# Optimization experiments

Hardware: AMD Instinct MI355X
Metric: run time of the kernel (lower is better)

## Reference

```python
import jax, jax.numpy as jnp
import numpy as np

N, D, E, TOP_K = 16384, 1024, 8, 2

def setup_inputs() -> dict:
    key = jax.random.key(0)
    ks = jax.random.split(key, 8)
    sc = 1.0 / np.sqrt(D)
    return {
        "x": jax.random.normal(ks[0], (N, D), dtype=jnp.float32),
        "context_vector": jax.random.uniform(ks[1], (E,), dtype=jnp.float32),
        "router_w": jax.random.uniform(ks[2], (E, D), minval=-sc, maxval=sc),
        "router_b": jax.random.uniform(ks[3], (E,), minval=-sc, maxval=sc),
        "expert_w": jax.random.uniform(ks[4], (E, D, D), minval=-sc, maxval=sc),
        "expert_b": jax.random.uniform(ks[5], (E, D), minval=-sc, maxval=sc),
        "context_weight": jax.random.uniform(ks[6], (1,), dtype=jnp.float32),
    }

def reference(x, context_vector, router_w, router_b, expert_w, expert_b, context_weight):
    # Router: gate logits with conceptual context bias. [N, E]
    gate_logits = x @ router_w.T + router_b + context_weight * context_vector
    weights = jax.nn.softmax(gate_logits, axis=-1)

    # Top-k selection and renormalization. [N, k]
    top_k_weights, top_k_indices = jax.lax.top_k(weights, TOP_K)
    top_k_weights = top_k_weights / jnp.sum(top_k_weights, axis=-1, keepdims=True)

    # All-expert outputs (dense grouped GEMM): y[n,e,:] = x[n] @ W[e].T + b[e]
    all_out = jnp.einsum('nd,efd->nef', x, expert_w) + expert_b  # [N, E, D]

    # Gather the top-k expert outputs per token and combine. [N, k, D]
    gathered = jnp.take_along_axis(all_out, top_k_indices[:, :, None], axis=1)
    expert_outputs = jnp.sum(top_k_weights[:, :, None] * gathered, axis=1)  # [N, D]

    # Load-balancing loss: avg router prob . fraction of tokens routed per expert
    avg_router_prob = weights.mean(axis=0)  # [E]
    assignment_mask = jax.nn.one_hot(top_k_indices, E).sum(axis=1)  # [N, E]
    fraction_routed = assignment_mask.mean(axis=0)  # [E]
    load_loss = jnp.sum(avg_router_prob * fraction_routed)

    return expert_outputs, load_loss
```

## Files before the change

### kernel.cpp

```cpp
#include <hip/hip_runtime.h>
#include <stdint.h>

#define N_TOK 16384
#define DDIM  1024
#define NEXP  8
#define CNT_STRIDE 64

#define BM 128
#define BN 128
#define BK 32

typedef __bf16 bf16x8 __attribute__((ext_vector_type(8)));
typedef float  f32x4  __attribute__((ext_vector_type(4)));

__device__ __forceinline__ unsigned short f2bf(float f) {
  union { float f; uint32_t u; } a; a.f = f;
  uint32_t u = a.u;
  u += 0x7fffu + ((u >> 16) & 1u);
  return (unsigned short)(u >> 16);
}

__device__ __forceinline__ float bf2f(unsigned short u) {
  union { uint32_t u; float f; } a; a.u = ((uint32_t)u) << 16;
  return a.f;
}

__device__ __forceinline__ void load_lds16(const void* g, void* l) {
  __builtin_amdgcn_global_load_lds(
      (const __attribute__((address_space(1))) void*)g,
      (__attribute__((address_space(3))) void*)l,
      16, 0, 0);
}

__global__ __launch_bounds__(256) void cast_w_kernel(const float4* __restrict__ src,
                                                     ushort4* __restrict__ dst) {
  size_t i = (size_t)blockIdx.x * 256 + threadIdx.x;
  float4 v = src[i];
  dst[i] = make_ushort4(f2bf(v.x), f2bf(v.y), f2bf(v.z), f2bf(v.w));
}

__global__ __launch_bounds__(256) void router_kernel(
    const float* __restrict__ x, const float* __restrict__ rw,
    const float* __restrict__ rb, const float* __restrict__ cv,
    const float* __restrict__ cwp,
    unsigned short* __restrict__ xg,
    int* __restrict__ perm_idx, float* __restrict__ perm_w,
    int* __restrict__ inv_idx,
    int* __restrict__ cnt, float* __restrict__ sum_w)
{
  __shared__ int   sCnt[NEXP];
  __shared__ int   sBase[NEXP];
  __shared__ float sSW[NEXP];
  __shared__ int   sE0[32], sE1[32], sR0[32], sR1[32];
  __shared__ float sW0[32], sW1[32];

  const int tid = threadIdx.x;
  if (tid < NEXP) { sCnt[tid] = 0; sSW[tid] = 0.0f; }
  __syncthreads();

  const int wave = tid >> 6;
  const int lane = tid & 63;

  float lsw[NEXP];
#pragma unroll
  for (int e = 0; e < NEXP; ++e) lsw[e] = 0.0f;

  const float cw = cwp[0];

  for (int t = 0; t < 8; ++t) {
    const int i = wave * 8 + t;
    const int n = blockIdx.x * 32 + i;

    float p[NEXP];
#pragma unroll
    for (int e = 0; e < NEXP; ++e) p[e] = 0.0f;

    const float2* x2 = (const float2*)(x + (size_t)n * DDIM);
    uint32_t* xgp = (uint32_t*)(xg + (size_t)n * DDIM);

    float2 xv[8];
#pragma unroll
    for (int it = 0; it < 8; ++it) xv[it] = x2[lane + 64 * it];
#pragma unroll
    for (int it = 0; it < 8; ++it) {
      int dp = lane + 64 * it;
      xgp[dp] = (uint32_t)f2bf(xv[it].x) | ((uint32_t)f2bf(xv[it].y) << 16);
#pragma unroll
      for (int e = 0; e < NEXP; ++e) {
        float2 wv = ((const float2*)(rw + e * DDIM))[dp];
        p[e] = fmaf(xv[it].x, wv.x, fmaf(xv[it].y, wv.y, p[e]));
      }
    }
#pragma unroll
    for (int e = 0; e < NEXP; ++e) {
#pragma unroll
      for (int off = 32; off > 0; off >>= 1)
        p[e] += __shfl_xor(p[e], off, 64);
    }

    if (lane == 0) {
      float w[NEXP];
      float m = -1e30f;
#pragma unroll
      for (int e = 0; e < NEXP; ++e) {
        w[e] = p[e] + rb[e] + cw * cv[e];
        m = fmaxf(m, w[e]);
      }
      float s = 0.0f;
#pragma unroll
      for (int e = 0; e < NEXP; ++e) { w[e] = expf(w[e] - m); s += w[e]; }
      float inv = 1.0f / s;
#pragma unroll
      for (int e = 0; e < NEXP; ++e) { w[e] *= inv; lsw[e] += w[e]; }
      int e0 = 0;
#pragma unroll
      for (int e = 1; e < NEXP; ++e) if (w[e] > w[e0]) e0 = e;
      int e1 = (e0 == 0) ? 1 : 0;
#pragma unroll
      for (int e = 0; e < NEXP; ++e) if (e != e0 && w[e] > w[e1]) e1 = e;
      float rsum = 1.0f / (w[e0] + w[e1]);
      int r0 = atomicAdd(&sCnt[e0], 1);
      int r1 = atomicAdd(&sCnt[e1], 1);
      sE0[i] = e0; sE1[i] = e1; sR0[i] = r0; sR1[i] = r1;
      sW0[i] = w[e0] * rsum; sW1[i] = w[e1] * rsum;
    }
  }

  if (lane == 0) {
#pragma unroll
    for (int e = 0; e < NEXP; ++e) atomicAdd(&sSW[e], lsw[e]);
  }
  __syncthreads();

  if (tid < NEXP) {
    sBase[tid] = atomicAdd(&cnt[tid * CNT_STRIDE], sCnt[tid]);
    atomicAdd(&sum_w[tid * CNT_STRIDE], sSW[tid]);
  }
  __syncthreads();

  if (tid < 64) {
    int i = tid >> 1, k = tid & 1;
    int e = k ? sE1[i] : sE0[i];
    int r = k ? sR1[i] : sR0[i];
    float wv = k ? sW1[i] : sW0[i];
    int pos = sBase[e] + r;
    int n = blockIdx.x * 32 + i;
    perm_idx[e * N_TOK + pos] = n;
    perm_w [e * N_TOK + pos] = wv;
    inv_idx[2 * n + k] = (e << 14) | pos;
  }
}

template<int MODE>
__global__ __launch_bounds__(256) void moe_gemm_kernel(
    const unsigned short* __restrict__ xg, const unsigned short* __restrict__ wb,
    const float* __restrict__ eb,
    const int* __restrict__ perm_idx, const float* __restrict__ perm_w,
    const int* __restrict__ cnt,
    unsigned short* __restrict__ ybuf, float* __restrict__ out)
{
  const int e = blockIdx.z;
  const int count = cnt[e * CNT_STRIDE];
  const int tm = blockIdx.x;
  if (tm * BM >= count) return;
  const int tn = blockIdx.y;

  __shared__ alignas(16) __bf16 As[BM * BK];
  __shared__ alignas(16) __bf16 Bs[BN * BK];
  __shared__ int   tokS[BM];
  __shared__ float wtS[BM];

  const int tid = threadIdx.x;
  const int wave = tid >> 6;
  const int lane = tid & 63;

  if (tid < BM) {
    int row = tm * BM + tid;
    int rc = row < count ? row : count - 1;
    tokS[tid] = perm_idx[e * N_TOK + rc];
    wtS[tid] = (row < count) ? perm_w[e * N_TOK + row] : 0.0f;
  }
  __syncthreads();

  const int slot = lane & 3;
  const int ar0 = wave * 32 + (lane >> 2);
  const int ar1 = ar0 + 16;
  const int ac0 = slot ^ ((ar0 >> 1) & 3);
  const int ac1 = slot ^ ((ar1 >> 1) & 3);

  const unsigned short* aptr0 = xg + (size_t)tokS[ar0] * DDIM + ac0 * 8;
  const unsigned short* aptr1 = xg + (size_t)tokS[ar1] * DDIM + ac1 * 8;
  const unsigned short* wbase = wb + (size_t)e * DDIM * DDIM;
  const unsigned short* bptr0 = wbase + (size_t)(tn * BN + ar0) * DDIM + ac0 * 8;
  const unsigned short* bptr1 = wbase + (size_t)(tn * BN + ar1) * DDIM + ac1 * 8;

  __bf16* aw0 = &As[(wave * 32) * BK];
  __bf16* aw1 = &As[(wave * 32 + 16) * BK];
  __bf16* bw0 = &Bs[(wave * 32) * BK];
  __bf16* bw1 = &Bs[(wave * 32 + 16) * BK];

  const int mw = (wave >> 1) * 64;
  const int nw = (wave & 1) * 64;
  const int quad = lane >> 4;
  const int l15 = lane & 15;

  f32x4 acc[4][4] = {};

  for (int kk = 0; kk < DDIM; kk += BK) {
    load_lds16(aptr0, aw0);
    load_lds16(aptr1, aw1);
    load_lds16(bptr0, bw0);
    load_lds16(bptr1, bw1);
    aptr0 += BK; aptr1 += BK; bptr0 += BK; bptr1 += BK;
    __syncthreads();

    bf16x8 af[4], bfr[4];
#pragma unroll
    for (int mi = 0; mi < 4; ++mi) {
      int m = mw + mi * 16 + l15;
      int pos = quad ^ ((m >> 1) & 3);
      af[mi] = *(const bf16x8*)&As[m * BK + pos * 8];
    }
#pragma unroll
    for (int ni = 0; ni < 4; ++ni) {
      int nn = nw + ni * 16 + l15;
      int pos = quad ^ ((nn >> 1) & 3);
      bfr[ni] = *(const bf16x8*)&Bs[nn * BK + pos * 8];
    }
#pragma unroll
    for (int mi = 0; mi < 4; ++mi)
#pragma unroll
      for (int ni = 0; ni < 4; ++ni)
        acc[mi][ni] = __builtin_amdgcn_mfma_f32_16x16x32_bf16(af[mi], bfr[ni], acc[mi][ni], 0, 0, 0);
    __syncthreads();
  }

  int ebase = 0;
  if (MODE == 1) {
#pragma unroll
    for (int j = 0; j < NEXP; ++j) if (j < e) ebase += cnt[j * CNT_STRIDE];
  }

  const int valid = count - tm * BM;
#pragma unroll
  for (int ni = 0; ni < 4; ++ni) {
    int col = tn * BN + nw + ni * 16 + l15;
    float bias = eb[e * DDIM + col];
#pragma unroll
    for (int mi = 0; mi < 4; ++mi) {
#pragma unroll
      for (int r = 0; r < 4; ++r) {
        int mrow = mw + mi * 16 + quad * 4 + r;
        if (mrow < valid) {
          float v = (acc[mi][ni][r] + bias) * wtS[mrow];
          if (MODE == 1) {
            ybuf[(size_t)(ebase + tm * BM + mrow) * DDIM + col] = f2bf(v);
          } else {
            atomicAdd(out + (size_t)tokS[mrow] * DDIM + col, v);
          }
        }
      }
    }
  }
}

__global__ __launch_bounds__(256) void combine_kernel(
    const unsigned short* __restrict__ ybuf, const int* __restrict__ inv_idx,
    const int* __restrict__ cnt, float* __restrict__ out)
{
  const int wave = threadIdx.x >> 6;
  const int lane = threadIdx.x & 63;
  const int n = blockIdx.x * 4 + wave;

  int base[NEXP];
  int acc = 0;
#pragma unroll
  for (int j = 0; j < NEXP; ++j) { base[j] = acc; acc += cnt[j * CNT_STRIDE]; }

  int i0 = inv_idx[2 * n];
  int i1 = inv_idx[2 * n + 1];
  int g0 = base[i0 >> 14] + (i0 & 16383);
  int g1 = base[i1 >> 14] + (i1 & 16383);

  const ushort4* r0 = (const ushort4*)(ybuf + (size_t)g0 * DDIM);
  const ushort4* r1 = (const ushort4*)(ybuf + (size_t)g1 * DDIM);
  float4* o = (float4*)(out + (size_t)n * DDIM);

#pragma unroll
  for (int it = 0; it < 4; ++it) {
    int c = lane + 64 * it;
    ushort4 a = r0[c];
    ushort4 b = r1[c];
    float4 v;
    v.x = bf2f(a.x) + bf2f(b.x);
    v.y = bf2f(a.y) + bf2f(b.y);
    v.z = bf2f(a.z) + bf2f(b.z);
    v.w = bf2f(a.w) + bf2f(b.w);
    o[c] = v;
  }
}

__global__ void loss_kernel(const float* __restrict__ sum_w,
                            const int* __restrict__ cnt,
                            float* __restrict__ out) {
  if (threadIdx.x == 0 && blockIdx.x == 0) {
    float l = 0.0f;
#pragma unroll
    for (int e = 0; e < NEXP; ++e)
      l += sum_w[e * CNT_STRIDE] * (float)cnt[e * CNT_STRIDE];
    out[(size_t)N_TOK * DDIM] = l * (1.0f / ((float)N_TOK * (float)N_TOK));
  }
}

extern "C" void kernel_launch(void* const* d_in, const int* in_sizes, int n_in,
                              void* d_out, int out_size, void* d_ws, size_t ws_size,
                              hipStream_t stream) {
  const float* x  = (const float*)d_in[0];
  const float* cv = (const float*)d_in[1];
  const float* rw = (const float*)d_in[2];
  const float* rb = (const float*)d_in[3];
  const float* ew = (const float*)d_in[4];
  const float* eb = (const float*)d_in[5];
  const float* cw = (const float*)d_in[6];
  float* out = (float*)d_out;

  char* ws = (char*)d_ws;
  unsigned short* xg = (unsigned short*)ws;
  unsigned short* wb = (unsigned short*)(ws + 33554432);
  int*   perm_idx = (int*)  (ws + 50331648);
  float* perm_w   = (float*)(ws + 50855936);
  int*   inv_idx  = (int*)  (ws + 51380224);
  int*   cnt      = (int*)  (ws + 51511296);
  float* sum_w    = (float*)(ws + 51513344);
  unsigned short* ybuf = (unsigned short*)(ws + 51515392);
  const size_t NEED = 51515392ull + 67108864ull;

  const bool big = ws_size >= NEED;

  hipMemsetAsync(cnt, 0, 4096, stream);
  if (!big)
    hipMemsetAsync(d_out, 0, (size_t)N_TOK * DDIM * sizeof(float), stream);

  cast_w_kernel<<<(NEXP * DDIM * DDIM / 4) / 256, 256, 0, stream>>>(
      (const float4*)ew, (ushort4*)wb);

  router_kernel<<<N_TOK / 32, 256, 0, stream>>>(x, rw, rb, cv, cw,
                                                xg, perm_idx, perm_w, inv_idx, cnt, sum_w);

  if (big) {
    moe_gemm_kernel<1><<<dim3(N_TOK / BM, DDIM / BN, NEXP), 256, 0, stream>>>(
        xg, wb, eb, perm_idx, perm_w, cnt, ybuf, out);
    combine_kernel<<<N_TOK / 4, 256, 0, stream>>>(ybuf, inv_idx, cnt, out);
  } else {
    moe_gemm_kernel<0><<<dim3(N_TOK / BM, DDIM / BN, NEXP), 256, 0, stream>>>(
        xg, wb, eb, perm_idx, perm_w, cnt, ybuf, out);
  }

  loss_kernel<<<1, 64, 0, stream>>>(sum_w, cnt, out);
}
```

Baseline: 321.9 us.

## Fuse weight cast into router, compact GEMM grid, BK=64, LDS-staged epilogue

Folds the expert-weight fp32→bf16 cast into the router kernel, which now runs 512 threads per block, so one launch is removed. The GEMM drops the 3D grid, where most blocks exited early, for a 1D grid over a prefix sum of per-expert tile counts. It also doubles BK to 64 with a new 8-way XOR swizzle, which halves the barrier count. The epilogue stages bf16 results in LDS for 16-byte coalesced stores, and the combine kernel uses wider 16-byte loads. The risks are higher LDS use, possible occupancy loss, and a MAX_TILES bound that assumes at most 264 M-tiles.

```diff
diff --git a/kernel.cpp b/kernel.cpp
--- a/kernel.cpp
+++ b/kernel.cpp
@@ -8,7 +8,9 @@
 
 #define BM 128
 #define BN 128
-#define BK 32
+#define BK 64
+#define MAX_TILES 264
+#define EP_PITCH 72
 
 typedef __bf16 bf16x8 __attribute__((ext_vector_type(8)));
 typedef float  f32x4  __attribute__((ext_vector_type(4)));
@@ -25,6 +27,12 @@
   return a.f;
 }
 
+__device__ __forceinline__ float2 bfpair(uint32_t u) {
+  union { uint32_t u; float f; } lo, hi;
+  lo.u = u << 16; hi.u = u & 0xffff0000u;
+  return make_float2(lo.f, hi.f);
+}
+
 __device__ __forceinline__ void load_lds16(const void* g, void* l) {
   __builtin_amdgcn_global_load_lds(
       (const __attribute__((address_space(1))) void*)g,
@@ -32,17 +40,11 @@
       16, 0, 0);
 }
 
-__global__ __launch_bounds__(256) void cast_w_kernel(const float4* __restrict__ src,
-                                                     ushort4* __restrict__ dst) {
-  size_t i = (size_t)blockIdx.x * 256 + threadIdx.x;
-  float4 v = src[i];
-  dst[i] = make_ushort4(f2bf(v.x), f2bf(v.y), f2bf(v.z), f2bf(v.w));
-}
-
-__global__ __launch_bounds__(256) void router_kernel(
+__global__ __launch_bounds__(512) void router_kernel(
     const float* __restrict__ x, const float* __restrict__ rw,
     const float* __restrict__ rb, const float* __restrict__ cv,
     const float* __restrict__ cwp,
+    const float4* __restrict__ ew4, ushort4* __restrict__ wb4,
     unsigned short* __restrict__ xg,
     int* __restrict__ perm_idx, float* __restrict__ perm_w,
     int* __restrict__ inv_idx,
@@ -67,8 +69,8 @@
 
   const float cw = cwp[0];
 
-  for (int t = 0; t < 8; ++t) {
-    const int i = wave * 8 + t;
+  for (int t = 0; t < 4; ++t) {
+    const int i = wave * 4 + t;
     const int n = blockIdx.x * 32 + i;
 
     float p[NEXP];
@@ -149,6 +151,14 @@
     perm_w [e * N_TOK + pos] = wv;
     inv_idx[2 * n + k] = (e << 14) | pos;
   }
+
+  size_t base = (size_t)blockIdx.x * 512 + tid;
+#pragma unroll
+  for (int i2 = 0; i2 < 8; ++i2) {
+    size_t idx = base + (size_t)i2 * 262144;
+    float4 v = ew4[idx];
+    wb4[idx] = make_ushort4(f2bf(v.x), f2bf(v.y), f2bf(v.z), f2bf(v.w));
+  }
 }
 
 template<int MODE>
@@ -159,14 +169,25 @@
     const int* __restrict__ cnt,
     unsigned short* __restrict__ ybuf, float* __restrict__ out)
 {
-  const int e = blockIdx.z;
-  const int count = cnt[e * CNT_STRIDE];
-  const int tm = blockIdx.x;
-  if (tm * BM >= count) return;
-  const int tn = blockIdx.y;
-
-  __shared__ alignas(16) __bf16 As[BM * BK];
-  __shared__ alignas(16) __bf16 Bs[BN * BK];
+  const int id = blockIdx.x;
+  const int tn = id / MAX_TILES;
+  const int tileIdx = id - tn * MAX_TILES;
+
+  int e = -1, tm = 0, count = 0, ebase = 0, pref = 0;
+#pragma unroll
+  for (int j = 0; j < NEXP; ++j) {
+    int c = cnt[j * CNT_STRIDE];
+    int t = (c + BM - 1) >> 7;
+    if (e < 0 && tileIdx < pref + t) { e = j; tm = tileIdx - pref; count = c; }
+    if (e < 0) ebase += c;
+    pref += t;
+  }
+  if (e < 0) return;
+
+  __shared__ union {
+    struct { __bf16 As[BM * BK]; __bf16 Bs[BN * BK]; } g;
+    __bf16 ep[4 * 64 * EP_PITCH];
+  } sm;
   __shared__ int   tokS[BM];
   __shared__ float wtS[BM];
 
@@ -182,22 +203,16 @@
   }
   __syncthreads();
 
-  const int slot = lane & 3;
-  const int ar0 = wave * 32 + (lane >> 2);
-  const int ar1 = ar0 + 16;
-  const int ac0 = slot ^ ((ar0 >> 1) & 3);
-  const int ac1 = slot ^ ((ar1 >> 1) & 3);
-
-  const unsigned short* aptr0 = xg + (size_t)tokS[ar0] * DDIM + ac0 * 8;
-  const unsigned short* aptr1 = xg + (size_t)tokS[ar1] * DDIM + ac1 * 8;
+  const unsigned short* aptr[4];
+  const unsigned short* bptr[4];
   const unsigned short* wbase = wb + (size_t)e * DDIM * DDIM;
-  const unsigned short* bptr0 = wbase + (size_t)(tn * BN + ar0) * DDIM + ac0 * 8;
-  const unsigned short* bptr1 = wbase + (size_t)(tn * BN + ar1) * DDIM + ac1 * 8;
-
-  __bf16* aw0 = &As[(wave * 32) * BK];
-  __bf16* aw1 = &As[(wave * 32 + 16) * BK];
-  __bf16* bw0 = &Bs[(wave * 32) * BK];
-  __bf16* bw1 = &Bs[(wave * 32 + 16) * BK];
+#pragma unroll
+  for (int t = 0; t < 4; ++t) {
+    int r = wave * 32 + t * 8 + (lane >> 3);
+    int cg = (lane & 7) ^ (r & 7);
+    aptr[t] = xg + (size_t)tokS[r] * DDIM + cg * 8;
+    bptr[t] = wbase + (size_t)(tn * BN + r) * DDIM + cg * 8;
+  }
 
   const int mw = (wave >> 1) * 64;
   const int nw = (wave & 1) * 64;
@@ -207,57 +222,81 @@
   f32x4 acc[4][4] = {};
 
   for (int kk = 0; kk < DDIM; kk += BK) {
-    load_lds16(aptr0, aw0);
-    load_lds16(aptr1, aw1);
-    load_lds16(bptr0, bw0);
-    load_lds16(bptr1, bw1);
-    aptr0 += BK; aptr1 += BK; bptr0 += BK; bptr1 += BK;
+#pragma unroll
+    for (int t = 0; t < 4; ++t) {
+      load_lds16(aptr[t], &sm.g.As[(wave * 32 + t * 8) * BK]);
+      load_lds16(bptr[t], &sm.g.Bs[(wave * 32 + t * 8) * BK]);
+      aptr[t] += BK; bptr[t] += BK;
+    }
     __syncthreads();
 
-    bf16x8 af[4], bfr[4];
+#pragma unroll
+    for (int ks = 0; ks < 2; ++ks) {
+      bf16x8 af[4], bfr[4];
+#pragma unroll
+      for (int mi = 0; mi < 4; ++mi) {
+        int m = mw + mi * 16 + l15;
+        int slot = (ks * 4 + quad) ^ (m & 7);
+        af[mi] = *(const bf16x8*)&sm.g.As[m * BK + slot * 8];
+      }
+#pragma unroll
+      for (int ni = 0; ni < 4; ++ni) {
+        int n = nw + ni * 16 + l15;
+        int slot = (ks * 4 + quad) ^ (n & 7);
+        bfr[ni] = *(const bf16x8*)&sm.g.Bs[n * BK + slot * 8];
+      }
+#pragma unroll
+      for (int mi = 0; mi < 4; ++mi)
+#pragma unroll
+        for (int ni = 0; ni < 4; ++ni)
+          acc[mi][ni] = __builtin_amdgcn_mfma_f32_16x16x32_bf16(bfr[ni], af[mi], acc[mi][ni], 0, 0, 0);
+    }
+    __syncthreads();
+  }
+
+  const int valid = count - tm * BM;
+
+  if (MODE == 1) {
+    __bf16* slab = &sm.ep[wave * (64 * EP_PITCH)];
 #pragma unroll
     for (int mi = 0; mi < 4; ++mi) {
-      int m = mw + mi * 16 + l15;
-      int pos = quad ^ ((m >> 1) & 3);
-      af[mi] = *(const bf16x8*)&As[m * BK + pos * 8];
-    }
-#pragma unroll
-    for (int ni = 0; ni < 4; ++ni) {
-      int nn = nw + ni * 16 + l15;
-      int pos = quad ^ ((nn >> 1) & 3);
-      bfr[ni] = *(const bf16x8*)&Bs[nn * BK + pos * 8];
-    }
-#pragma unroll
-    for (int mi = 0; mi < 4; ++mi)
-#pragma unroll
-      for (int ni = 0; ni < 4; ++ni)
-        acc[mi][ni] = __builtin_amdgcn_mfma_f32_16x16x32_bf16(af[mi], bfr[ni], acc[mi][ni], 0, 0, 0);
-    __syncthreads();
-  }
-
-  int ebase = 0;
-  if (MODE == 1) {
-#pragma unroll
-    for (int j = 0; j < NEXP; ++j) if (j < e) ebase += cnt[j * CNT_STRIDE];
-  }
-
-  const int valid = count - tm * BM;
-#pragma unroll
-  for (int ni = 0; ni < 4; ++ni) {
-    int col = tn * BN + nw + ni * 16 + l15;
-    float bias = eb[e * DDIM + col];
+      float wt = wtS[mw + mi * 16 + l15];
+#pragma unroll
+      for (int ni = 0; ni < 4; ++ni) {
+        int gcol = tn * BN + nw + ni * 16 + quad * 4;
+        const float4 bv = *(const float4*)&eb[e * DDIM + gcol];
+        ushort4 pk;
+        pk.x = f2bf((acc[mi][ni][0] + bv.x) * wt);
+        pk.y = f2bf((acc[mi][ni][1] + bv.y) * wt);
+        pk.z = f2bf((acc[mi][ni][2] + bv.z) * wt);
+        pk.w = f2bf((acc[mi][ni][3] + bv.w) * wt);
+        *(ushort4*)&slab[(mi * 16 + l15) * EP_PITCH + ni * 16 + quad * 4] = pk;
+      }
+    }
+    const int gb = ebase + tm * BM;
+#pragma unroll
+    for (int s = 0; s < 8; ++s) {
+      int lrow = s * 8 + (lane >> 3);
+      uint4 v = *(const uint4*)&slab[lrow * EP_PITCH + (lane & 7) * 8];
+      int brow = mw + lrow;
+      if (brow < valid)
+        *(uint4*)&ybuf[(size_t)(gb + brow) * DDIM + tn * BN + nw + (lane & 7) * 8] = v;
+    }
+  } else {
 #pragma unroll
     for (int mi = 0; mi < 4; ++mi) {
-#pragma unroll
-      for (int r = 0; r < 4; ++r) {
-        int mrow = mw + mi * 16 + quad * 4 + r;
-        if (mrow < valid) {
-          float v = (acc[mi][ni][r] + bias) * wtS[mrow];
-          if (MODE == 1) {
-            ybuf[(size_t)(ebase + tm * BM + mrow) * DDIM + col] = f2bf(v);
-          } else {
-            atomicAdd(out + (size_t)tokS[mrow] * DDIM + col, v);
-          }
+      int brow = mw + mi * 16 + l15;
+      float wt = wtS[brow];
+      int tok = tokS[brow];
+#pragma unroll
+      for (int ni = 0; ni < 4; ++ni) {
+        int gcol = tn * BN + nw + ni * 16 + quad * 4;
+        const float4 bv = *(const float4*)&eb[e * DDIM + gcol];
+        if (brow < valid) {
+          atomicAdd(out + (size_t)tok * DDIM + gcol + 0, (acc[mi][ni][0] + bv.x) * wt);
+          atomicAdd(out + (size_t)tok * DDIM + gcol + 1, (acc[mi][ni][1] + bv.y) * wt);
+          atomicAdd(out + (size_t)tok * DDIM + gcol + 2, (acc[mi][ni][2] + bv.z) * wt);
+          atomicAdd(out + (size_t)tok * DDIM + gcol + 3, (acc[mi][ni][3] + bv.w) * wt);
         }
       }
     }
@@ -282,21 +321,22 @@
   int g0 = base[i0 >> 14] + (i0 & 16383);
   int g1 = base[i1 >> 14] + (i1 & 16383);
 
-  const ushort4* r0 = (const ushort4*)(ybuf + (size_t)g0 * DDIM);
-  const ushort4* r1 = (const ushort4*)(ybuf + (size_t)g1 * DDIM);
+  const uint4* r0 = (const uint4*)(ybuf + (size_t)g0 * DDIM);
+  const uint4* r1 = (const uint4*)(ybuf + (size_t)g1 * DDIM);
   float4* o = (float4*)(out + (size_t)n * DDIM);
 
 #pragma unroll
-  for (int it = 0; it < 4; ++it) {
+  for (int it = 0; it < 2; ++it) {
     int c = lane + 64 * it;
-    ushort4 a = r0[c];
-    ushort4 b = r1[c];
-    float4 v;
-    v.x = bf2f(a.x) + bf2f(b.x);
-    v.y = bf2f(a.y) + bf2f(b.y);
-    v.z = bf2f(a.z) + bf2f(b.z);
-    v.w = bf2f(a.w) + bf2f(b.w);
-    o[c] = v;
+    uint4 a = r0[c];
+    uint4 b = r1[c];
+    float2 a0 = bfpair(a.x), a1 = bfpair(a.y), a2 = bfpair(a.z), a3 = bfpair(a.w);
+    float2 b0 = bfpair(b.x), b1 = bfpair(b.y), b2 = bfpair(b.z), b3 = bfpair(b.w);
+    float4 v0, v1;
+    v0.x = a0.x + b0.x; v0.y = a0.y + b0.y; v0.z = a1.x + b1.x; v0.w = a1.y + b1.y;
+    v1.x = a2.x + b2.x; v1.y = a2.y + b2.y; v1.z = a3.x + b3.x; v1.w = a3.y + b3.y;
+    o[2 * c] = v0;
+    o[2 * c + 1] = v1;
   }
 }
 
@@ -341,18 +381,16 @@
   if (!big)
     hipMemsetAsync(d_out, 0, (size_t)N_TOK * DDIM * sizeof(float), stream);
 
-  cast_w_kernel<<<(NEXP * DDIM * DDIM / 4) / 256, 256, 0, stream>>>(
-      (const float4*)ew, (ushort4*)wb);
-
-  router_kernel<<<N_TOK / 32, 256, 0, stream>>>(x, rw, rb, cv, cw,
+  router_kernel<<<N_TOK / 32, 512, 0, stream>>>(x, rw, rb, cv, cw,
+                                                (const float4*)ew, (ushort4*)wb,
                                                 xg, perm_idx, perm_w, inv_idx, cnt, sum_w);
 
   if (big) {
-    moe_gemm_kernel<1><<<dim3(N_TOK / BM, DDIM / BN, NEXP), 256, 0, stream>>>(
+    moe_gemm_kernel<1><<<MAX_TILES * 8, 256, 0, stream>>>(
         xg, wb, eb, perm_idx, perm_w, cnt, ybuf, out);
     combine_kernel<<<N_TOK / 4, 256, 0, stream>>>(ybuf, inv_idx, cnt, out);
   } else {
-    moe_gemm_kernel<0><<<dim3(N_TOK / BM, DDIM / BN, NEXP), 256, 0, stream>>>(
+    moe_gemm_kernel<0><<<MAX_TILES * 8, 256, 0, stream>>>(
         xg, wb, eb, perm_idx, perm_w, cnt, ybuf, out);
   }
 
```

Result: faster. 292.0 us (-9.3%).
